# Performance work log

Measured on AMD Instinct MI355X. Metric: run time of the kernel, lower is better.

Reference implementation:

```python
import jax, jax.numpy as jnp
import numpy as np
from jax import lax

B = 128
ROUTING_ITER = 3
EPS = 1e-9


def _conv(x, w, b, stride):
    y = lax.conv_general_dilated(x, w, window_strides=(stride, stride), padding='VALID',
                                 dimension_numbers=('NCHW', 'OIHW', 'NCHW'))
    return y + b[None, :, None, None]


def _squash(s):
    # squash along capsule dim (axis=3), s: [B,1,10,16,1]
    sq = jnp.sum(s * s, axis=3, keepdims=True)
    return (sq / (1.0 + sq)) * s / jnp.sqrt(sq + EPS)


def setup_inputs() -> dict:
    key = jax.random.key(0)
    ks = jax.random.split(key, 16)
    x = jax.random.normal(ks[0], (B, 1, 28, 28), dtype=jnp.float32)
    labels = jax.random.randint(ks[1], (B,), 0, 10)
    y = jax.nn.one_hot(labels, 10, dtype=jnp.float32)
    conv1_w = jax.random.normal(ks[2], (256, 1, 9, 9), dtype=jnp.float32) * 0.05
    conv1_b = jnp.zeros((256,), dtype=jnp.float32)
    caps1_w = jax.random.normal(ks[3], (256, 256, 9, 9), dtype=jnp.float32) * 0.01
    caps1_b = jnp.zeros((256,), dtype=jnp.float32)
    W = jax.random.normal(ks[4], (1, 1152, 10, 8, 16), dtype=jnp.float32) * 0.05
    caps_bias = jnp.zeros((1, 1, 10, 16, 1), dtype=jnp.float32)
    fc1_w = jax.random.normal(ks[5], (512, 16), dtype=jnp.float32) * 0.1
    fc1_b = jnp.zeros((512,), dtype=jnp.float32)
    fc2_w = jax.random.normal(ks[6], (1024, 512), dtype=jnp.float32) * 0.04
    fc2_b = jnp.zeros((1024,), dtype=jnp.float32)
    fc3_w = jax.random.normal(ks[7], (784, 1024), dtype=jnp.float32) * 0.03
    fc3_b = jnp.zeros((784,), dtype=jnp.float32)
    return {'x': x, 'y': y, 'conv1_w': conv1_w, 'conv1_b': conv1_b,
            'caps1_w': caps1_w, 'caps1_b': caps1_b, 'W': W, 'caps_bias': caps_bias,
            'fc1_w': fc1_w, 'fc1_b': fc1_b, 'fc2_w': fc2_w, 'fc2_b': fc2_b,
            'fc3_w': fc3_w, 'fc3_b': fc3_b}


def _forward(x, y, conv1_w, conv1_b, caps1_w, caps1_b, W, caps_bias,
             fc1_w, fc1_b, fc2_w, fc2_b, fc3_w, fc3_b):
    h = jax.nn.relu(_conv(x, conv1_w, conv1_b, 1))          # [B,256,20,20]
    h = jax.nn.relu(_conv(h, caps1_w, caps1_b, 2))          # [B,256,6,6]

    # faithful repeat+view layout from the torch code (NOT a transpose)
    x_view = jnp.tile(h.reshape(B, 256, 1, 6, 6), (1, 1, 10, 1, 1)).reshape(B, 1152, 10, 8, 1)
    W_view = jnp.broadcast_to(W, (B, 1152, 10, 8, 16)).reshape(B, 1152, 10, 16, 8)
    u_hat = jnp.matmul(W_view, x_view)                      # [B,1152,10,16,1]
    u_hat_stopped = lax.stop_gradient(u_hat)

    b_ij = jnp.zeros((B, 1152, 10, 1, 1), dtype=u_hat.dtype)
    V_J = None
    for r in range(ROUTING_ITER):
        c_ij = jax.nn.softmax(b_ij, axis=2)                 # softmax over 10 classes
        if r < ROUTING_ITER - 1:
            s_j = jnp.sum(c_ij * u_hat_stopped, axis=1, keepdims=True) + caps_bias
            v_j = _squash(s_j)                              # [B,1,10,16,1]
            # agreement: u_hat^T . v, [B,1152,10,1,16] @ [B,1152,10,16,1]
            agree = jnp.matmul(u_hat_stopped.reshape(B, 1152, 10, 1, 16),
                               jnp.broadcast_to(v_j, (B, 1152, 10, 16, 1)))
            b_ij = b_ij + agree
        else:
            s_j = jnp.sum(c_ij * u_hat, axis=1, keepdims=True) + caps_bias
            V_J = _squash(s_j)                              # [B,1,10,16,1]

    caps_out = jnp.squeeze(V_J, axis=1)                     # [B,10,16,1]
    v_length = jnp.sqrt(jnp.sum(caps_out * caps_out, axis=2, keepdims=True) + EPS)
    v_length = v_length.reshape(B, 10, 1, 1)

    # torch: squeeze -> [B,10,16], then .view(B,16,10) (reshape, not transpose)
    flat = caps_out.reshape(B, 10, 16).reshape(B, 16, 10)
    masked_v = jnp.matmul(flat, y.reshape(B, 10, 1)).reshape(B, 16)

    fc1 = masked_v @ fc1_w.T + fc1_b                        # no activation (faithful)
    fc2 = fc1 @ fc2_w.T + fc2_b
    reconstruction = jax.nn.sigmoid(fc2 @ fc3_w.T + fc3_b)  # [B,784]
    return v_length, reconstruction


def reference(x, y, conv1_w, conv1_b, caps1_w, caps1_b, W, caps_bias,
              fc1_w, fc1_b, fc2_w, fc2_b, fc3_w, fc3_b):
    return _forward(x, y, conv1_w, conv1_b, caps1_w, caps1_b, W, caps_bias,
                    fc1_w, fc1_b, fc2_w, fc2_b, fc3_w, fc3_b)
```

## Files before the change

### kernel.cpp

```cpp
#include <hip/hip_runtime.h>
#include <hip/hip_bf16.h>

typedef unsigned short ushort_t;
typedef __attribute__((ext_vector_type(8))) short short8;
typedef __attribute__((ext_vector_type(4))) float f32x4;


#define OFFB_H1T  0u
#define OFFB_WT   26214400u
#define OFFB_PART 36831232u
#define OFFB_H2   55705600u
#define OFFB_UH   60424192u
#define OFFB_BIJ  107610112u
#define OFFB_C    113508352u
#define OFFB_V    119406592u
#define OFFB_F1   119488512u
#define OFFB_F2   119750656u
#define OFFB_W1T  120274944u

__device__ __forceinline__ ushort_t f2bf(float f) {
  union { float f; unsigned int u; } c; c.f = f;
  unsigned int r = (c.u + 0x7FFFu + ((c.u >> 16) & 1u)) >> 16;
  return (ushort_t)r;
}
__device__ __forceinline__ float bf2f(ushort_t u) {
  union { unsigned int i; float f; } c; c.i = ((unsigned int)u) << 16;
  return c.f;
}

__global__ __launch_bounds__(256) void w1t_kernel(
    const float* __restrict__ w, float* __restrict__ w1t) {
  int kk = blockIdx.x;
  int co = threadIdx.x;
  w1t[kk * 256 + co] = w[co * 81 + kk];
}

__global__ __launch_bounds__(256) void conv1_kernel(
    const float* __restrict__ x, const float* __restrict__ w1t,
    const float* __restrict__ bias, ushort_t* __restrict__ h1t) {
  int blk = blockIdx.x;
  int b = blk / 20, oy = blk % 20;
  int co = threadIdx.x;
  __shared__ float xs[252];
  for (int l = co; l < 252; l += 256)
    xs[l] = x[b * 784 + (oy + l / 28) * 28 + (l % 28)];
  __syncthreads();
  float bs = bias[co];
  float acc[20];
#pragma unroll
  for (int i = 0; i < 20; ++i) acc[i] = bs;
  for (int ky = 0; ky < 9; ++ky) {
    float xr[28];
#pragma unroll
    for (int i = 0; i < 28; ++i) xr[i] = xs[ky * 28 + i];
    float wk[9];
#pragma unroll
    for (int kx = 0; kx < 9; ++kx) wk[kx] = w1t[(ky * 9 + kx) * 256 + co];
#pragma unroll
    for (int kx = 0; kx < 9; ++kx)
#pragma unroll
      for (int ox = 0; ox < 20; ++ox) acc[ox] += wk[kx] * xr[ox + kx];
  }
  int xb = (b * 20 + oy) * 20;
#pragma unroll
  for (int ox = 0; ox < 20; ++ox)
    h1t[(xb + ox) * 256 + co] = f2bf(fmaxf(acc[ox], 0.f));
}

__global__ __launch_bounds__(256) void wreorder_kernel(
    const float* __restrict__ w, ushort_t* __restrict__ wt) {
  int co = blockIdx.x;
  __shared__ ushort_t wl[256 * 82];
  int t = threadIdx.x;
  const float* src = w + (size_t)co * 20736;
  for (int e = t; e < 20736; e += 256) {
    int ci = e / 81, kk = e - ci * 81;
    wl[ci * 82 + kk] = f2bf(src[e]);
  }
  __syncthreads();
  for (int kk = 0; kk < 81; ++kk)
    wt[((size_t)kk * 256 + co) * 256 + t] = wl[t * 82 + kk];
}

__global__ __launch_bounds__(512) void caps1_gemm(
    const ushort_t* __restrict__ h1t, const ushort_t* __restrict__ wt,
    float* __restrict__ part) {
  int lb = (blockIdx.x & 7) * 72 + (blockIdx.x >> 3);
  int chunk = lb / 144;
  int tile = lb - chunk * 144;
  int gm0 = (tile >> 2) * 128;
  int gn0 = (tile & 3) * 64;
  int ci0 = chunk << 6;
  int t = threadIdx.x;
  int wave = t >> 6, lane = t & 63;
  int wm = (wave >> 1) * 32, wn = (wave & 1) * 32;
  int lr = lane & 15, lg = lane >> 4;

  __shared__ __align__(16) ushort_t As[2][128 * 64];
  __shared__ __align__(16) ushort_t Bs[2][64 * 64];

  int ar = t >> 2, aseg = t & 3;
  int am = gm0 + ar;
  int ab_ = am / 36, pos = am - ab_ * 36;
  int oy = pos / 6, ox = pos - oy * 6;
  const ushort_t* arow =
      h1t + ((ab_ * 20 + 2 * oy) * 20 + 2 * ox) * 256 + ci0 + aseg * 16;
  int ax = ar & 7;
  int ast0 = ar * 64 + (((aseg << 1) | 0) ^ ax) * 8;
  int ast1 = ar * 64 + (((aseg << 1) | 1) ^ ax) * 8;
  int brr = t >> 3, bseg = t & 7;
  const ushort_t* brow = wt + (size_t)(gn0 + brr) * 256 + ci0 + bseg * 8;
  int bst = brr * 64 + (bseg ^ (brr & 7)) * 8;

  int lx = lr & 7;
  int sl0 = ((0 * 4 + lg) ^ lx) * 8;
  int sl1 = ((1 * 4 + lg) ^ lx) * 8;

  f32x4 acc[2][2];
#pragma unroll
  for (int i = 0; i < 2; ++i)
#pragma unroll
    for (int j = 0; j < 2; ++j)
#pragma unroll
      for (int e = 0; e < 4; ++e) acc[i][j][e] = 0.f;

  float4 ra0, ra1, rb0;
  ra0 = *(const float4*)(arow);
  ra1 = *(const float4*)(arow + 8);
  rb0 = *(const float4*)(brow);
  *(float4*)&As[0][ast0] = ra0;
  *(float4*)&As[0][ast1] = ra1;
  *(float4*)&Bs[0][bst] = rb0;
  __syncthreads();

  int buf = 0;
  for (int kk = 0; kk < 81; ++kk) {
    int nxt = kk + 1;
    if (nxt < 81) {
      int ky = nxt / 9, kx = nxt - ky * 9;
      const ushort_t* ap = arow + (ky * 20 + kx) * 256;
      ra0 = *(const float4*)(ap);
      ra1 = *(const float4*)(ap + 8);
      rb0 = *(const float4*)(brow + (size_t)nxt * 65536);
    }
    short8 af[2][2], bfr[2][2];
#pragma unroll
    for (int mf = 0; mf < 2; ++mf) {
      int ra = (wm + mf * 16 + lr) * 64;
      af[mf][0] = *(const short8*)&As[buf][ra + sl0];
      af[mf][1] = *(const short8*)&As[buf][ra + sl1];
    }
#pragma unroll
    for (int nf = 0; nf < 2; ++nf) {
      int rb = (wn + nf * 16 + lr) * 64;
      bfr[nf][0] = *(const short8*)&Bs[buf][rb + sl0];
      bfr[nf][1] = *(const short8*)&Bs[buf][rb + sl1];
    }
#pragma unroll
    for (int kh = 0; kh < 2; ++kh)
#pragma unroll
      for (int mf = 0; mf < 2; ++mf)
#pragma unroll
        for (int nf = 0; nf < 2; ++nf)
          acc[mf][nf] = __builtin_amdgcn_mfma_f32_16x16x32_bf16(
              af[mf][kh], bfr[nf][kh], acc[mf][nf], 0, 0, 0);
    __syncthreads();
    if (nxt < 81) {
      int nb = buf ^ 1;
      *(float4*)&As[nb][ast0] = ra0;
      *(float4*)&As[nb][ast1] = ra1;
      *(float4*)&Bs[nb][bst] = rb0;
      __syncthreads();
    }
    buf ^= 1;
  }

  float* pbase = part + (size_t)chunk * 4608 * 256;
#pragma unroll
  for (int mf = 0; mf < 2; ++mf)
#pragma unroll
    for (int nf = 0; nf < 2; ++nf) {
      int nn = gn0 + wn + nf * 16 + lr;
#pragma unroll
      for (int reg = 0; reg < 4; ++reg) {
        int mm = gm0 + wm + mf * 16 + lg * 4 + reg;
        pbase[(size_t)mm * 256 + nn] = acc[mf][nf][reg];
      }
    }
}

__global__ __launch_bounds__(256) void reduce_kernel(
    const float* __restrict__ part, const float* __restrict__ bias,
    float* __restrict__ h2) {
  int m = blockIdx.x;
  int n = threadIdx.x;
  size_t o = (size_t)m * 256 + n;
  float s = part[o] + part[o + 4608 * 256] + part[o + 2 * 4608 * 256] +
            part[o + 3 * 4608 * 256];
  h2[o] = fmaxf(s + bias[n], 0.f);
}

__global__ __launch_bounds__(256) void uhat_kernel(
    const float* __restrict__ h2, const float* __restrict__ W,
    ushort_t* __restrict__ uh) {
  int blk = blockIdx.x;
  int bh = blk & 1;
  int qpc = blk >> 1;
  int q = qpc / 72;
  int pc = qpc - q * 72;
  int p0 = pc * 16;
  int b0 = bh * 64;
  __shared__ float Wl[16][132];
  __shared__ float xl[64][16][9];
  int t = threadIdx.x;
#pragma unroll
  for (int it = 0; it < 2; ++it) {
    int idx = t * 2 + it;
    int row = idx >> 5;
    int c4 = idx & 31;
    float4 vv = *(reinterpret_cast<const float4*>(
        &W[(size_t)((p0 + row) * 10 + q) * 128]) + c4);
    Wl[row][c4 * 4 + 0] = vv.x;
    Wl[row][c4 * 4 + 1] = vv.y;
    Wl[row][c4 * 4 + 2] = vv.z;
    Wl[row][c4 * 4 + 3] = vv.w;
  }
  for (int j = 0; j < 32; ++j) {
    int e = t + 256 * j;
    int b_l = e >> 7;
    int rem = e & 127;
    int i = rem >> 3, n = rem & 7;
    int f = (p0 + i) * 80 + q * 8 + n;
    xl[b_l][i][n] = h2[((size_t)(b0 + b_l) * 36 + (f % 36)) * 256 + (f / 360)];
  }
  __syncthreads();
  int p_l = t & 15;
  int b_ll = t >> 4;
  const float* wr = &Wl[p_l][0];
#pragma unroll
  for (int k = 0; k < 4; ++k) {
    int b_l = b_ll + 16 * k;
    float xv[8];
#pragma unroll
    for (int n = 0; n < 8; ++n) xv[n] = xl[b_l][p_l][n];
    short8 o0, o1;
#pragma unroll
    for (int a = 0; a < 8; ++a) {
      float ue = 0.f, uo = 0.f;
#pragma unroll
      for (int n = 0; n < 8; ++n) {
        ue += wr[a * 16 + n] * xv[n];
        uo += wr[a * 16 + 8 + n] * xv[n];
      }
      if (a < 4) { o0[2 * a] = (short)f2bf(ue); o0[2 * a + 1] = (short)f2bf(uo); }
      else { o1[2 * (a - 4)] = (short)f2bf(ue); o1[2 * (a - 4) + 1] = (short)f2bf(uo); }
    }
    size_t dst = ((size_t)((b0 + b_l) * 10 + q) * 1152 + p0 + p_l) * 16;
    *(short8*)&uh[dst] = o0;
    *(short8*)&uh[dst + 8] = o1;
  }
}

template <int MODE>
__global__ __launch_bounds__(256) void sv_kernel(
    const ushort_t* __restrict__ uh, const float* __restrict__ cbuf,
    const float* __restrict__ caps_bias, float* __restrict__ v,
    float* __restrict__ out) {
  int bq = blockIdx.x;
  int q = bq % 10;
  int t = threadIdx.x;
  const ushort_t* ub = &uh[(size_t)bq * 1152 * 16];
  const float* cb = &cbuf[(size_t)bq * 1152];
  float s[16];
#pragma unroll
  for (int m = 0; m < 16; ++m) s[m] = 0.f;
  for (int p = t; p < 1152; p += 256) {
    short8 u0 = *(const short8*)&ub[p * 16];
    short8 u1 = *(const short8*)&ub[p * 16 + 8];
    float c = (MODE == 0) ? 0.1f : cb[p];
#pragma unroll
    for (int m = 0; m < 8; ++m) s[m] += c * bf2f((ushort_t)u0[m]);
#pragma unroll
    for (int m = 0; m < 8; ++m) s[8 + m] += c * bf2f((ushort_t)u1[m]);
  }
  __shared__ float red[4][16];
#pragma unroll
  for (int m = 0; m < 16; ++m) {
    float val = s[m];
#pragma unroll
    for (int off = 32; off > 0; off >>= 1) val += __shfl_down(val, off);
    if ((t & 63) == 0) red[t >> 6][m] = val;
  }
  __syncthreads();
  if (t == 0) {
    float sq = 0.f;
    float sj[16];
#pragma unroll
    for (int m = 0; m < 16; ++m) {
      sj[m] = red[0][m] + red[1][m] + red[2][m] + red[3][m] +
              caps_bias[q * 16 + m];
      sq += sj[m] * sj[m];
    }
    float coef = (sq / (1.f + sq)) * rsqrtf(sq + 1e-9f);
    float vl2 = 0.f;
#pragma unroll
    for (int m = 0; m < 16; ++m) {
      float vv = coef * sj[m];
      v[bq * 16 + m] = vv;
      vl2 += vv * vv;
    }
    if (MODE == 2) out[bq] = sqrtf(vl2 + 1e-9f);
  }
}

template <bool FIRST>
__global__ __launch_bounds__(256) void agree_kernel(
    const ushort_t* __restrict__ uh, const float* __restrict__ v,
    float* __restrict__ bij, float* __restrict__ cbuf) {
  int tid = blockIdx.x * 256 + threadIdx.x;
  int b = tid / 1152;
  int p = tid - b * 1152;
  float br[10];
  float* bp = &bij[(size_t)tid * 10];
#pragma unroll
  for (int q = 0; q < 10; ++q) {
    const ushort_t* ub = &uh[(size_t)((b * 10 + q) * 1152 + p) * 16];
    short8 u0 = *(const short8*)ub;
    short8 u1 = *(const short8*)(ub + 8);
    const float4* v4 = reinterpret_cast<const float4*>(&v[(b * 10 + q) * 16]);
    float4 b0 = v4[0], b1 = v4[1], b2 = v4[2], b3 = v4[3];
    float d = bf2f((ushort_t)u0[0]) * b0.x + bf2f((ushort_t)u0[1]) * b0.y
            + bf2f((ushort_t)u0[2]) * b0.z + bf2f((ushort_t)u0[3]) * b0.w
            + bf2f((ushort_t)u0[4]) * b1.x + bf2f((ushort_t)u0[5]) * b1.y
            + bf2f((ushort_t)u0[6]) * b1.z + bf2f((ushort_t)u0[7]) * b1.w
            + bf2f((ushort_t)u1[0]) * b2.x + bf2f((ushort_t)u1[1]) * b2.y
            + bf2f((ushort_t)u1[2]) * b2.z + bf2f((ushort_t)u1[3]) * b2.w
            + bf2f((ushort_t)u1[4]) * b3.x + bf2f((ushort_t)u1[5]) * b3.y
            + bf2f((ushort_t)u1[6]) * b3.z + bf2f((ushort_t)u1[7]) * b3.w;
    br[q] = (FIRST ? 0.f : bp[q]) + d;
  }
  float mx = br[0];
#pragma unroll
  for (int q = 1; q < 10; ++q) mx = fmaxf(mx, br[q]);
  float den = 0.f;
  float ex[10];
#pragma unroll
  for (int q = 0; q < 10; ++q) { ex[q] = __expf(br[q] - mx); den += ex[q]; }
  float inv = 1.f / den;
#pragma unroll
  for (int q = 0; q < 10; ++q) {
    bp[q] = br[q];
    cbuf[(size_t)(b * 10 + q) * 1152 + p] = ex[q] * inv;
  }
}

__global__ __launch_bounds__(128) void fc1_kernel(
    const float* __restrict__ v, const float* __restrict__ y,
    const float* __restrict__ fc1_w, const float* __restrict__ fc1_b,
    float* __restrict__ f1g) {
  int b = blockIdx.x, t = threadIdx.x;
  __shared__ float mv[16];
  if (t < 16) {
    const float* vb = &v[b * 160];
    float a = 0.f;
#pragma unroll
    for (int tt = 0; tt < 10; ++tt) a += vb[t * 10 + tt] * y[b * 10 + tt];
    mv[t] = a;
  }
  __syncthreads();
  for (int o = t; o < 512; o += 128) {
    const float4* wr = reinterpret_cast<const float4*>(&fc1_w[o * 16]);
    float4 w0 = wr[0], w1 = wr[1], w2 = wr[2], w3 = wr[3];
    f1g[b * 512 + o] = fc1_b[o]
        + mv[0] * w0.x + mv[1] * w0.y + mv[2] * w0.z + mv[3] * w0.w
        + mv[4] * w1.x + mv[5] * w1.y + mv[6] * w1.z + mv[7] * w1.w
        + mv[8] * w2.x + mv[9] * w2.y + mv[10] * w2.z + mv[11] * w2.w
        + mv[12] * w3.x + mv[13] * w3.y + mv[14] * w3.z + mv[15] * w3.w;
  }
}

__global__ __launch_bounds__(256) void fc2_kernel(
    const float* __restrict__ f1g, const float* __restrict__ fc2_w,
    const float* __restrict__ fc2_b, float* __restrict__ f2g) {
  int b = blockIdx.x >> 2;
  int o = (blockIdx.x & 3) * 256 + threadIdx.x;
  __shared__ float f1[512];
  for (int l = threadIdx.x; l < 512; l += 256) f1[l] = f1g[b * 512 + l];
  __syncthreads();
  const float4* wr = reinterpret_cast<const float4*>(&fc2_w[o * 512]);
  float a = fc2_b[o];
#pragma unroll 4
  for (int k4 = 0; k4 < 128; ++k4) {
    float4 w4 = wr[k4];
    a += f1[4 * k4] * w4.x + f1[4 * k4 + 1] * w4.y + f1[4 * k4 + 2] * w4.z +
         f1[4 * k4 + 3] * w4.w;
  }
  f2g[b * 1024 + o] = a;
}

__global__ __launch_bounds__(256) void fc3_kernel(
    const float* __restrict__ f2g, const float* __restrict__ fc3_w,
    const float* __restrict__ fc3_b, float* __restrict__ out) {
  int b = blockIdx.x >> 2;
  int oc = (blockIdx.x & 3) * 196;
  __shared__ float f2[1024];
  for (int l = threadIdx.x; l < 1024; l += 256) f2[l] = f2g[b * 1024 + l];
  __syncthreads();
  if (threadIdx.x >= 196) return;
  int o = oc + threadIdx.x;
  const float4* wr = reinterpret_cast<const float4*>(&fc3_w[o * 1024]);
  float a = fc3_b[o];
#pragma unroll 4
  for (int k4 = 0; k4 < 256; ++k4) {
    float4 w4 = wr[k4];
    a += f2[4 * k4] * w4.x + f2[4 * k4 + 1] * w4.y + f2[4 * k4 + 2] * w4.z +
         f2[4 * k4 + 3] * w4.w;
  }
  out[1280 + b * 784 + o] = 1.f / (1.f + __expf(-a));
}

extern "C" void kernel_launch(void* const* d_in, const int* in_sizes, int n_in,
                              void* d_out, int out_size, void* d_ws, size_t ws_size,
                              hipStream_t stream) {
  const float* x       = (const float*)d_in[0];
  const float* y       = (const float*)d_in[1];
  const float* conv1_w = (const float*)d_in[2];
  const float* conv1_b = (const float*)d_in[3];
  const float* caps1_w = (const float*)d_in[4];
  const float* caps1_b = (const float*)d_in[5];
  const float* W       = (const float*)d_in[6];
  const float* cbias   = (const float*)d_in[7];
  const float* fc1_w   = (const float*)d_in[8];
  const float* fc1_b   = (const float*)d_in[9];
  const float* fc2_w   = (const float*)d_in[10];
  const float* fc2_b   = (const float*)d_in[11];
  const float* fc3_w   = (const float*)d_in[12];
  const float* fc3_b   = (const float*)d_in[13];
  float* out = (float*)d_out;

  char* wsb = (char*)d_ws;
  ushort_t* h1t  = (ushort_t*)(wsb + OFFB_H1T);
  ushort_t* wt   = (ushort_t*)(wsb + OFFB_WT);
  float*    part = (float*)(wsb + OFFB_PART);
  float*    h2   = (float*)(wsb + OFFB_H2);
  ushort_t* uh   = (ushort_t*)(wsb + OFFB_UH);
  float*    bij  = (float*)(wsb + OFFB_BIJ);
  float*    c    = (float*)(wsb + OFFB_C);
  float*    v    = (float*)(wsb + OFFB_V);
  float*    f1   = (float*)(wsb + OFFB_F1);
  float*    f2   = (float*)(wsb + OFFB_F2);
  float*    w1t  = (float*)(wsb + OFFB_W1T);

  w1t_kernel<<<81, 256, 0, stream>>>(conv1_w, w1t);
  conv1_kernel<<<2560, 256, 0, stream>>>(x, w1t, conv1_b, h1t);
  wreorder_kernel<<<256, 256, 0, stream>>>(caps1_w, wt);
  caps1_gemm<<<576, 512, 0, stream>>>(h1t, wt, part);
  reduce_kernel<<<4608, 256, 0, stream>>>(part, caps1_b, h2);
  uhat_kernel<<<1440, 256, 0, stream>>>(h2, W, uh);

  sv_kernel<0><<<1280, 256, 0, stream>>>(uh, c, cbias, v, out);
  agree_kernel<true><<<576, 256, 0, stream>>>(uh, v, bij, c);
  sv_kernel<1><<<1280, 256, 0, stream>>>(uh, c, cbias, v, out);
  agree_kernel<false><<<576, 256, 0, stream>>>(uh, v, bij, c);
  sv_kernel<2><<<1280, 256, 0, stream>>>(uh, c, cbias, v, out);

  fc1_kernel<<<128, 128, 0, stream>>>(v, y, fc1_w, fc1_b, f1);
  fc2_kernel<<<512, 256, 0, stream>>>(f1, fc2_w, fc2_b, f2);
  fc3_kernel<<<512, 256, 0, stream>>>(f2, fc3_w, fc3_b, out);
}
```

Baseline: 330.6 us.

## Enlarge caps1 GEMM tiles to 128x128 per block and vectorize split-K reduce

The caps1 implicit GEMM now uses 128x128 output tiles with 4 waves, each computing a 64x64 sub-tile (4x4 MFMA fragments), in place of 128x64 tiles with 8 waves at 32x32. The grid halves to 288 blocks. The aim is more operand reuse per LDS read and less global traffic for A and B, at the cost of more accumulator registers, fewer waves per block, and a grid of 288 blocks that may underfill the 256 CUs. The split-K reduce kernel now handles four floats per thread with float4 loads and stores.

```diff
diff --git a/kernel.cpp b/kernel.cpp
--- a/kernel.cpp
+++ b/kernel.cpp
@@ -82,55 +82,59 @@
     wt[((size_t)kk * 256 + co) * 256 + t] = wl[t * 82 + kk];
 }
 
-__global__ __launch_bounds__(512) void caps1_gemm(
+__global__ __launch_bounds__(256) void caps1_gemm(
     const ushort_t* __restrict__ h1t, const ushort_t* __restrict__ wt,
     float* __restrict__ part) {
-  int lb = (blockIdx.x & 7) * 72 + (blockIdx.x >> 3);
-  int chunk = lb / 144;
-  int tile = lb - chunk * 144;
-  int gm0 = (tile >> 2) * 128;
-  int gn0 = (tile & 3) * 64;
+  int lb = (blockIdx.x & 7) * 36 + (blockIdx.x >> 3);
+  int chunk = lb / 72;
+  int tile = lb - chunk * 72;
+  int gm0 = (tile >> 1) * 128;
+  int gn0 = (tile & 1) * 128;
   int ci0 = chunk << 6;
   int t = threadIdx.x;
   int wave = t >> 6, lane = t & 63;
-  int wm = (wave >> 1) * 32, wn = (wave & 1) * 32;
+  int wm = (wave >> 1) * 64, wn = (wave & 1) * 64;
   int lr = lane & 15, lg = lane >> 4;
 
   __shared__ __align__(16) ushort_t As[2][128 * 64];
-  __shared__ __align__(16) ushort_t Bs[2][64 * 64];
-
-  int ar = t >> 2, aseg = t & 3;
-  int am = gm0 + ar;
+  __shared__ __align__(16) ushort_t Bs[2][128 * 64];
+
+  int row = t >> 1;
+  int cib = (t & 1) * 32;
+  int am = gm0 + row;
   int ab_ = am / 36, pos = am - ab_ * 36;
   int oy = pos / 6, ox = pos - oy * 6;
   const ushort_t* arow =
-      h1t + ((ab_ * 20 + 2 * oy) * 20 + 2 * ox) * 256 + ci0 + aseg * 16;
-  int ax = ar & 7;
-  int ast0 = ar * 64 + (((aseg << 1) | 0) ^ ax) * 8;
-  int ast1 = ar * 64 + (((aseg << 1) | 1) ^ ax) * 8;
-  int brr = t >> 3, bseg = t & 7;
-  const ushort_t* brow = wt + (size_t)(gn0 + brr) * 256 + ci0 + bseg * 8;
-  int bst = brr * 64 + (bseg ^ (brr & 7)) * 8;
-
+      h1t + ((ab_ * 20 + 2 * oy) * 20 + 2 * ox) * 256 + ci0 + cib;
+  const ushort_t* brow = wt + (size_t)(gn0 + row) * 256 + ci0 + cib;
+  int rx = row & 7;
+  int st[4];
+#pragma unroll
+  for (int j = 0; j < 4; ++j)
+    st[j] = row * 64 + ((((t & 1) * 4 + j)) ^ rx) * 8;
   int lx = lr & 7;
   int sl0 = ((0 * 4 + lg) ^ lx) * 8;
   int sl1 = ((1 * 4 + lg) ^ lx) * 8;
 
-  f32x4 acc[2][2];
-#pragma unroll
-  for (int i = 0; i < 2; ++i)
-#pragma unroll
-    for (int j = 0; j < 2; ++j)
+  f32x4 acc[4][4];
+#pragma unroll
+  for (int i = 0; i < 4; ++i)
+#pragma unroll
+    for (int j = 0; j < 4; ++j)
 #pragma unroll
       for (int e = 0; e < 4; ++e) acc[i][j][e] = 0.f;
 
-  float4 ra0, ra1, rb0;
-  ra0 = *(const float4*)(arow);
-  ra1 = *(const float4*)(arow + 8);
-  rb0 = *(const float4*)(brow);
-  *(float4*)&As[0][ast0] = ra0;
-  *(float4*)&As[0][ast1] = ra1;
-  *(float4*)&Bs[0][bst] = rb0;
+  float4 ra[4], rb[4];
+#pragma unroll
+  for (int j = 0; j < 4; ++j) {
+    ra[j] = *(const float4*)(arow + j * 8);
+    rb[j] = *(const float4*)(brow + j * 8);
+  }
+#pragma unroll
+  for (int j = 0; j < 4; ++j) {
+    *(float4*)&As[0][st[j]] = ra[j];
+    *(float4*)&Bs[0][st[j]] = rb[j];
+  }
   __syncthreads();
 
   int buf = 0;
@@ -139,37 +143,42 @@
     if (nxt < 81) {
       int ky = nxt / 9, kx = nxt - ky * 9;
       const ushort_t* ap = arow + (ky * 20 + kx) * 256;
-      ra0 = *(const float4*)(ap);
-      ra1 = *(const float4*)(ap + 8);
-      rb0 = *(const float4*)(brow + (size_t)nxt * 65536);
-    }
-    short8 af[2][2], bfr[2][2];
-#pragma unroll
-    for (int mf = 0; mf < 2; ++mf) {
-      int ra = (wm + mf * 16 + lr) * 64;
-      af[mf][0] = *(const short8*)&As[buf][ra + sl0];
-      af[mf][1] = *(const short8*)&As[buf][ra + sl1];
-    }
-#pragma unroll
-    for (int nf = 0; nf < 2; ++nf) {
-      int rb = (wn + nf * 16 + lr) * 64;
-      bfr[nf][0] = *(const short8*)&Bs[buf][rb + sl0];
-      bfr[nf][1] = *(const short8*)&Bs[buf][rb + sl1];
+      const ushort_t* bp = brow + (size_t)nxt * 65536;
+#pragma unroll
+      for (int j = 0; j < 4; ++j) {
+        ra[j] = *(const float4*)(ap + j * 8);
+        rb[j] = *(const float4*)(bp + j * 8);
+      }
+    }
+    short8 af[4][2], bfr[4][2];
+#pragma unroll
+    for (int mf = 0; mf < 4; ++mf) {
+      int raoff = (wm + mf * 16 + lr) * 64;
+      af[mf][0] = *(const short8*)&As[buf][raoff + sl0];
+      af[mf][1] = *(const short8*)&As[buf][raoff + sl1];
+    }
+#pragma unroll
+    for (int nf = 0; nf < 4; ++nf) {
+      int rboff = (wn + nf * 16 + lr) * 64;
+      bfr[nf][0] = *(const short8*)&Bs[buf][rboff + sl0];
+      bfr[nf][1] = *(const short8*)&Bs[buf][rboff + sl1];
     }
 #pragma unroll
     for (int kh = 0; kh < 2; ++kh)
 #pragma unroll
-      for (int mf = 0; mf < 2; ++mf)
-#pragma unroll
-        for (int nf = 0; nf < 2; ++nf)
+      for (int mf = 0; mf < 4; ++mf)
+#pragma unroll
+        for (int nf = 0; nf < 4; ++nf)
           acc[mf][nf] = __builtin_amdgcn_mfma_f32_16x16x32_bf16(
               af[mf][kh], bfr[nf][kh], acc[mf][nf], 0, 0, 0);
     __syncthreads();
     if (nxt < 81) {
       int nb = buf ^ 1;
-      *(float4*)&As[nb][ast0] = ra0;
-      *(float4*)&As[nb][ast1] = ra1;
-      *(float4*)&Bs[nb][bst] = rb0;
+#pragma unroll
+      for (int j = 0; j < 4; ++j) {
+        *(float4*)&As[nb][st[j]] = ra[j];
+        *(float4*)&Bs[nb][st[j]] = rb[j];
+      }
       __syncthreads();
     }
     buf ^= 1;
@@ -177,9 +186,9 @@
 
   float* pbase = part + (size_t)chunk * 4608 * 256;
 #pragma unroll
-  for (int mf = 0; mf < 2; ++mf)
-#pragma unroll
-    for (int nf = 0; nf < 2; ++nf) {
+  for (int mf = 0; mf < 4; ++mf)
+#pragma unroll
+    for (int nf = 0; nf < 4; ++nf) {
       int nn = gn0 + wn + nf * 16 + lr;
 #pragma unroll
       for (int reg = 0; reg < 4; ++reg) {
@@ -192,12 +201,20 @@
 __global__ __launch_bounds__(256) void reduce_kernel(
     const float* __restrict__ part, const float* __restrict__ bias,
     float* __restrict__ h2) {
-  int m = blockIdx.x;
-  int n = threadIdx.x;
-  size_t o = (size_t)m * 256 + n;
-  float s = part[o] + part[o + 4608 * 256] + part[o + 2 * 4608 * 256] +
-            part[o + 3 * 4608 * 256];
-  h2[o] = fmaxf(s + bias[n], 0.f);
+  int tid = blockIdx.x * 256 + threadIdx.x;
+  size_t o = (size_t)tid * 4;
+  int n0 = (int)(o & 255);
+  float4 s0 = *(const float4*)&part[o];
+  float4 s1 = *(const float4*)&part[o + (size_t)4608 * 256];
+  float4 s2 = *(const float4*)&part[o + (size_t)2 * 4608 * 256];
+  float4 s3 = *(const float4*)&part[o + (size_t)3 * 4608 * 256];
+  float4 bv = *(const float4*)&bias[n0];
+  float4 r;
+  r.x = fmaxf(s0.x + s1.x + s2.x + s3.x + bv.x, 0.f);
+  r.y = fmaxf(s0.y + s1.y + s2.y + s3.y + bv.y, 0.f);
+  r.z = fmaxf(s0.z + s1.z + s2.z + s3.z + bv.z, 0.f);
+  r.w = fmaxf(s0.w + s1.w + s2.w + s3.w + bv.w, 0.f);
+  *(float4*)&h2[o] = r;
 }
 
 __global__ __launch_bounds__(256) void uhat_kernel(
@@ -454,8 +471,8 @@
   w1t_kernel<<<81, 256, 0, stream>>>(conv1_w, w1t);
   conv1_kernel<<<2560, 256, 0, stream>>>(x, w1t, conv1_b, h1t);
   wreorder_kernel<<<256, 256, 0, stream>>>(caps1_w, wt);
-  caps1_gemm<<<576, 512, 0, stream>>>(h1t, wt, part);
-  reduce_kernel<<<4608, 256, 0, stream>>>(part, caps1_b, h2);
+  caps1_gemm<<<288, 256, 0, stream>>>(h1t, wt, part);
+  reduce_kernel<<<1152, 256, 0, stream>>>(part, caps1_b, h2);
   uhat_kernel<<<1440, 256, 0, stream>>>(h2, W, uh);
 
   sv_kernel<0><<<1280, 256, 0, stream>>>(uh, c, cbias, v, out);
```

New measurement: 485.0 us. +46.7%, slower.

## Fuse dynamic routing iterations into one per-batch kernel with LDS state

Applied to the files above, without the earlier changes.

Replaces the five separate sv/agree launches with a single route_kernel that runs all three routing iterations per batch element in one 512-thread block, keeping b_ij and c_ij in shared memory instead of global buffers. This removes launch overhead and the global round-trips for b_ij and c. In exchange only 128 blocks run, on a GPU with many more CUs, and each block reads u_hat serially several times, so parallelism drops sharply. The reduce kernel is also vectorised to float4 loads and stores with a quarter as many blocks.

```diff
diff --git a/kernel.cpp b/kernel.cpp
--- a/kernel.cpp
+++ b/kernel.cpp
@@ -11,12 +11,10 @@
 #define OFFB_PART 36831232u
 #define OFFB_H2   55705600u
 #define OFFB_UH   60424192u
-#define OFFB_BIJ  107610112u
-#define OFFB_C    113508352u
-#define OFFB_V    119406592u
-#define OFFB_F1   119488512u
-#define OFFB_F2   119750656u
-#define OFFB_W1T  120274944u
+#define OFFB_V    107610112u
+#define OFFB_F1   107692032u
+#define OFFB_F2   107954176u
+#define OFFB_W1T  108478464u
 
 __device__ __forceinline__ ushort_t f2bf(float f) {
   union { float f; unsigned int u; } c; c.f = f;
@@ -192,12 +190,20 @@
 __global__ __launch_bounds__(256) void reduce_kernel(
     const float* __restrict__ part, const float* __restrict__ bias,
     float* __restrict__ h2) {
-  int m = blockIdx.x;
-  int n = threadIdx.x;
-  size_t o = (size_t)m * 256 + n;
-  float s = part[o] + part[o + 4608 * 256] + part[o + 2 * 4608 * 256] +
-            part[o + 3 * 4608 * 256];
-  h2[o] = fmaxf(s + bias[n], 0.f);
+  int tid = blockIdx.x * 256 + threadIdx.x;
+  size_t o = (size_t)tid * 4;
+  int n0 = (int)(o & 255);
+  float4 s0 = *(const float4*)&part[o];
+  float4 s1 = *(const float4*)&part[o + (size_t)4608 * 256];
+  float4 s2 = *(const float4*)&part[o + (size_t)2 * 4608 * 256];
+  float4 s3 = *(const float4*)&part[o + (size_t)3 * 4608 * 256];
+  float4 bv = *(const float4*)&bias[n0];
+  float4 r;
+  r.x = fmaxf(s0.x + s1.x + s2.x + s3.x + bv.x, 0.f);
+  r.y = fmaxf(s0.y + s1.y + s2.y + s3.y + bv.y, 0.f);
+  r.z = fmaxf(s0.z + s1.z + s2.z + s3.z + bv.z, 0.f);
+  r.w = fmaxf(s0.w + s1.w + s2.w + s3.w + bv.w, 0.f);
+  *(float4*)&h2[o] = r;
 }
 
 __global__ __launch_bounds__(256) void uhat_kernel(
@@ -261,96 +267,100 @@
   }
 }
 
-template <int MODE>
-__global__ __launch_bounds__(256) void sv_kernel(
-    const ushort_t* __restrict__ uh, const float* __restrict__ cbuf,
-    const float* __restrict__ caps_bias, float* __restrict__ v,
-    float* __restrict__ out) {
-  int bq = blockIdx.x;
-  int q = bq % 10;
+__global__ __launch_bounds__(512) void route_kernel(
+    const ushort_t* __restrict__ uh, const float* __restrict__ caps_bias,
+    float* __restrict__ v, float* __restrict__ out) {
+  int b = blockIdx.x;
   int t = threadIdx.x;
-  const ushort_t* ub = &uh[(size_t)bq * 1152 * 16];
-  const float* cb = &cbuf[(size_t)bq * 1152];
-  float s[16];
-#pragma unroll
-  for (int m = 0; m < 16; ++m) s[m] = 0.f;
-  for (int p = t; p < 1152; p += 256) {
-    short8 u0 = *(const short8*)&ub[p * 16];
-    short8 u1 = *(const short8*)&ub[p * 16 + 8];
-    float c = (MODE == 0) ? 0.1f : cb[p];
-#pragma unroll
-    for (int m = 0; m < 8; ++m) s[m] += c * bf2f((ushort_t)u0[m]);
-#pragma unroll
-    for (int m = 0; m < 8; ++m) s[8 + m] += c * bf2f((ushort_t)u1[m]);
-  }
-  __shared__ float red[4][16];
-#pragma unroll
-  for (int m = 0; m < 16; ++m) {
-    float val = s[m];
-#pragma unroll
-    for (int off = 32; off > 0; off >>= 1) val += __shfl_down(val, off);
-    if ((t & 63) == 0) red[t >> 6][m] = val;
-  }
-  __syncthreads();
-  if (t == 0) {
-    float sq = 0.f;
-    float sj[16];
-#pragma unroll
-    for (int m = 0; m < 16; ++m) {
-      sj[m] = red[0][m] + red[1][m] + red[2][m] + red[3][m] +
-              caps_bias[q * 16 + m];
-      sq += sj[m] * sj[m];
-    }
-    float coef = (sq / (1.f + sq)) * rsqrtf(sq + 1e-9f);
-    float vl2 = 0.f;
-#pragma unroll
-    for (int m = 0; m < 16; ++m) {
-      float vv = coef * sj[m];
-      v[bq * 16 + m] = vv;
-      vl2 += vv * vv;
-    }
-    if (MODE == 2) out[bq] = sqrtf(vl2 + 1e-9f);
-  }
-}
-
-template <bool FIRST>
-__global__ __launch_bounds__(256) void agree_kernel(
-    const ushort_t* __restrict__ uh, const float* __restrict__ v,
-    float* __restrict__ bij, float* __restrict__ cbuf) {
-  int tid = blockIdx.x * 256 + threadIdx.x;
-  int b = tid / 1152;
-  int p = tid - b * 1152;
-  float br[10];
-  float* bp = &bij[(size_t)tid * 10];
-#pragma unroll
-  for (int q = 0; q < 10; ++q) {
-    const ushort_t* ub = &uh[(size_t)((b * 10 + q) * 1152 + p) * 16];
-    short8 u0 = *(const short8*)ub;
-    short8 u1 = *(const short8*)(ub + 8);
-    const float4* v4 = reinterpret_cast<const float4*>(&v[(b * 10 + q) * 16]);
-    float4 b0 = v4[0], b1 = v4[1], b2 = v4[2], b3 = v4[3];
-    float d = bf2f((ushort_t)u0[0]) * b0.x + bf2f((ushort_t)u0[1]) * b0.y
-            + bf2f((ushort_t)u0[2]) * b0.z + bf2f((ushort_t)u0[3]) * b0.w
-            + bf2f((ushort_t)u0[4]) * b1.x + bf2f((ushort_t)u0[5]) * b1.y
-            + bf2f((ushort_t)u0[6]) * b1.z + bf2f((ushort_t)u0[7]) * b1.w
-            + bf2f((ushort_t)u1[0]) * b2.x + bf2f((ushort_t)u1[1]) * b2.y
-            + bf2f((ushort_t)u1[2]) * b2.z + bf2f((ushort_t)u1[3]) * b2.w
-            + bf2f((ushort_t)u1[4]) * b3.x + bf2f((ushort_t)u1[5]) * b3.y
-            + bf2f((ushort_t)u1[6]) * b3.z + bf2f((ushort_t)u1[7]) * b3.w;
-    br[q] = (FIRST ? 0.f : bp[q]) + d;
-  }
-  float mx = br[0];
-#pragma unroll
-  for (int q = 1; q < 10; ++q) mx = fmaxf(mx, br[q]);
-  float den = 0.f;
-  float ex[10];
-#pragma unroll
-  for (int q = 0; q < 10; ++q) { ex[q] = __expf(br[q] - mx); den += ex[q]; }
-  float inv = 1.f / den;
-#pragma unroll
-  for (int q = 0; q < 10; ++q) {
-    bp[q] = br[q];
-    cbuf[(size_t)(b * 10 + q) * 1152 + p] = ex[q] * inv;
+  __shared__ float bijl[1152 * 11];
+  __shared__ float cl[1152 * 11];
+  __shared__ float vsh[10][16];
+  __shared__ float red[8][16];
+  for (int i = t; i < 1152 * 11; i += 512) bijl[i] = 0.f;
+  __syncthreads();
+  const ushort_t* ub = uh + (size_t)b * 11520 * 16;
+
+  for (int r = 0; r < 3; ++r) {
+    if (r > 0) {
+      for (int q = 0; q < 10; ++q) {
+        float vq[16];
+#pragma unroll
+        for (int m = 0; m < 16; ++m) vq[m] = vsh[q][m];
+        for (int p = t; p < 1152; p += 512) {
+          const ushort_t* up = ub + ((size_t)q * 1152 + p) * 16;
+          short8 u0 = *(const short8*)up;
+          short8 u1 = *(const short8*)(up + 8);
+          float d = 0.f;
+#pragma unroll
+          for (int m = 0; m < 8; ++m) d += bf2f((ushort_t)u0[m]) * vq[m];
+#pragma unroll
+          for (int m = 0; m < 8; ++m) d += bf2f((ushort_t)u1[m]) * vq[8 + m];
+          bijl[p * 11 + q] += d;
+        }
+      }
+      __syncthreads();
+      for (int p = t; p < 1152; p += 512) {
+        float bv[10], mx = -1e30f;
+#pragma unroll
+        for (int q = 0; q < 10; ++q) {
+          bv[q] = bijl[p * 11 + q];
+          mx = fmaxf(mx, bv[q]);
+        }
+        float den = 0.f, ex[10];
+#pragma unroll
+        for (int q = 0; q < 10; ++q) { ex[q] = __expf(bv[q] - mx); den += ex[q]; }
+        float inv = 1.f / den;
+#pragma unroll
+        for (int q = 0; q < 10; ++q) cl[p * 11 + q] = ex[q] * inv;
+      }
+      __syncthreads();
+    }
+    for (int q = 0; q < 10; ++q) {
+      float s[16];
+#pragma unroll
+      for (int m = 0; m < 16; ++m) s[m] = 0.f;
+      for (int p = t; p < 1152; p += 512) {
+        const ushort_t* up = ub + ((size_t)q * 1152 + p) * 16;
+        short8 u0 = *(const short8*)up;
+        short8 u1 = *(const short8*)(up + 8);
+        float c = (r == 0) ? 0.1f : cl[p * 11 + q];
+#pragma unroll
+        for (int m = 0; m < 8; ++m) s[m] += c * bf2f((ushort_t)u0[m]);
+#pragma unroll
+        for (int m = 0; m < 8; ++m) s[8 + m] += c * bf2f((ushort_t)u1[m]);
+      }
+#pragma unroll
+      for (int m = 0; m < 16; ++m) {
+        float val = s[m];
+#pragma unroll
+        for (int off = 32; off > 0; off >>= 1) val += __shfl_down(val, off);
+        if ((t & 63) == 0) red[t >> 6][m] = val;
+      }
+      __syncthreads();
+      if (t == 0) {
+        float sj[16], sq = 0.f;
+#pragma unroll
+        for (int m = 0; m < 16; ++m) {
+          sj[m] = red[0][m] + red[1][m] + red[2][m] + red[3][m] + red[4][m] +
+                  red[5][m] + red[6][m] + red[7][m] + caps_bias[q * 16 + m];
+          sq += sj[m] * sj[m];
+        }
+        float coef = (sq / (1.f + sq)) * rsqrtf(sq + 1e-9f);
+        float vl2 = 0.f;
+#pragma unroll
+        for (int m = 0; m < 16; ++m) {
+          float vv = coef * sj[m];
+          vsh[q][m] = vv;
+          vl2 += vv * vv;
+        }
+        if (r == 2) {
+#pragma unroll
+          for (int m = 0; m < 16; ++m) v[(b * 10 + q) * 16 + m] = vsh[q][m];
+          out[b * 10 + q] = sqrtf(vl2 + 1e-9f);
+        }
+      }
+      __syncthreads();
+    }
   }
 }
 
@@ -444,8 +454,6 @@
   float*    part = (float*)(wsb + OFFB_PART);
   float*    h2   = (float*)(wsb + OFFB_H2);
   ushort_t* uh   = (ushort_t*)(wsb + OFFB_UH);
-  float*    bij  = (float*)(wsb + OFFB_BIJ);
-  float*    c    = (float*)(wsb + OFFB_C);
   float*    v    = (float*)(wsb + OFFB_V);
   float*    f1   = (float*)(wsb + OFFB_F1);
   float*    f2   = (float*)(wsb + OFFB_F2);
@@ -455,14 +463,10 @@
   conv1_kernel<<<2560, 256, 0, stream>>>(x, w1t, conv1_b, h1t);
   wreorder_kernel<<<256, 256, 0, stream>>>(caps1_w, wt);
   caps1_gemm<<<576, 512, 0, stream>>>(h1t, wt, part);
-  reduce_kernel<<<4608, 256, 0, stream>>>(part, caps1_b, h2);
+  reduce_kernel<<<1152, 256, 0, stream>>>(part, caps1_b, h2);
   uhat_kernel<<<1440, 256, 0, stream>>>(h2, W, uh);
 
-  sv_kernel<0><<<1280, 256, 0, stream>>>(uh, c, cbias, v, out);
-  agree_kernel<true><<<576, 256, 0, stream>>>(uh, v, bij, c);
-  sv_kernel<1><<<1280, 256, 0, stream>>>(uh, c, cbias, v, out);
-  agree_kernel<false><<<576, 256, 0, stream>>>(uh, v, bij, c);
-  sv_kernel<2><<<1280, 256, 0, stream>>>(uh, c, cbias, v, out);
+  route_kernel<<<128, 512, 0, stream>>>(uh, cbias, v, out);
 
   fc1_kernel<<<128, 128, 0, stream>>>(v, y, fc1_w, fc1_b, f1);
   fc2_kernel<<<512, 256, 0, stream>>>(f1, fc2_w, fc2_b, f2);
```

Measured after the change: 427.1 us. +29.2%, slower.
